# Kernel optimization log

Hardware: AMD Instinct MI355X
Metric: run time of the kernel (lower is better)

## Reference

```python
import jax, jax.numpy as jnp
import numpy as np

HISTORY = 64
WINDOW = 32
DIM = 32
N_PATTERNS = 16
AMP = 2.0


def setup_inputs() -> dict:
    key = jax.random.key(0)
    ks = jax.random.split(key, 7)
    B, L = 128, 131072
    T = L // WINDOW  # 4096 scan steps
    x = jax.random.normal(ks[0], (B, L), jnp.float32)
    avg = jax.random.normal(ks[1], (B, N_PATTERNS), jnp.float32)
    avg_scores = avg - avg.mean(axis=-1, keepdims=True)
    noise = jax.random.normal(ks[2], (B, T, WINDOW), jnp.float32)
    # keys: xavier_uniform on (dim, n_patterns)
    kbound = float(np.sqrt(6.0 / (DIM + N_PATTERNS)))
    keys = jax.random.uniform(ks[3], (DIM, N_PATTERNS), jnp.float32, -kbound, kbound)
    # shapes = rand(n_patterns, 2) * amp * 2
    shapes = jax.random.uniform(ks[4], (N_PATTERNS, 2), jnp.float32) * (AMP * 2.0)
    # conv1d default init: uniform(-1/sqrt(fan_in), 1/sqrt(fan_in)), fan_in = 1*history
    cb = float(1.0 / np.sqrt(HISTORY))
    conv_w = jax.random.uniform(ks[5], (DIM, 1, HISTORY), jnp.float32, -cb, cb)
    conv_b = jax.random.uniform(ks[6], (DIM,), jnp.float32, -cb, cb)
    return {"x": x, "avg_scores": avg_scores, "noise": noise,
            "conv_w": conv_w, "conv_b": conv_b, "keys": keys, "shapes": shapes}


def reference(x, avg_scores, noise, conv_w, conv_b, keys, shapes):
    B, L = x.shape
    inv_p = 1.0 / N_PATTERNS
    # left-pad by history-1, conv1d(1 -> dim, kernel=history, stride=window) + relu
    padded = jnp.pad(x, ((0, 0), (HISTORY - 1, 0)))[:, None, :]  # [B,1,L+H-1]
    out = jax.lax.conv_general_dilated(
        padded, conv_w, window_strides=(WINDOW,), padding='VALID',
        dimension_numbers=('NCH', 'OIH', 'NCH'))  # [B,dim,T]
    out = jax.nn.relu(out + conv_b[None, :, None])
    out = out.transpose(2, 0, 1)  # [T,B,dim]
    # relu6 attention scores against pattern keys
    attn_scores = jnp.clip(jnp.einsum('tbd,dp->tbp', out, keys), 0.0, 6.0)  # [T,B,P]

    def step(avg, score):
        prob = jax.nn.softmax(score - avg, axis=-1)  # [B,P]
        return avg + prob - inv_p, prob

    _, probs = jax.lax.scan(step, avg_scores, attn_scores)  # probs: [T,B,P]
    attn_probs = probs.transpose(1, 0, 2)  # [B,T,P]
    shapeparams = jnp.einsum('btp,pc->btc', attn_probs, shapes)  # [B,T,2]
    offset = shapeparams[:, :, 0:1]  # broadcast over window
    std = shapeparams[:, :, 1:2]
    signal = (offset + noise * std).reshape(B, -1)[:, :L]  # [B,L]
    return jax.nn.relu(signal - x)
```

## Files before the change

### kernel.cpp

```cpp
#include <hip/hip_runtime.h>

static constexpr int BATCH = 128;
static constexpr int LEN   = 131072;
static constexpr int T     = 4096;
static constexpr int DIM   = 32;
static constexpr int NP    = 16;

static constexpr int NCHUNK = 128;
static constexpr int SPC    = T / NCHUNK;
static constexpr int WARM   = 96;

static constexpr int TT = 128;

#define L2E   1.44269504088896340736f
#define L2E16 (1.44269504088896340736f / 16.0f)

typedef __attribute__((ext_vector_type(8))) short  short8;
typedef __attribute__((ext_vector_type(4))) float  f32x4;

__device__ __forceinline__ float fexp2(float x) {
#if __has_builtin(__builtin_amdgcn_exp2f)
  return __builtin_amdgcn_exp2f(x);
#else
  return exp2f(x);
#endif
}

__device__ __forceinline__ float frcp(float x) {
#if __has_builtin(__builtin_amdgcn_rcpf)
  return __builtin_amdgcn_rcpf(x);
#else
  return 1.0f / x;
#endif
}

template <int CTRL>
__device__ __forceinline__ float dppf(float v) {
  return __int_as_float(
      __builtin_amdgcn_update_dpp(0, __float_as_int(v), CTRL, 0xf, 0xf, true));
}

__device__ __forceinline__ float sum16(float v) {
  v += dppf<0xB1>(v);
  v += dppf<0x4E>(v);
  v += dppf<0x141>(v);
  v += dppf<0x140>(v);
  return v;
}

__device__ __forceinline__ short bf16c(float f) {
  unsigned u = __float_as_uint(f);
  unsigned r = u + 0x7fffu + ((u >> 16) & 1u);
  return (short)(r >> 16);
}

__global__ void __launch_bounds__(64) prep_kernel(
    const float* __restrict__ conv_w, const float* __restrict__ conv_b,
    const float* __restrict__ keys, short* __restrict__ frags) {
  int l = threadIdx.x;
  int ln15 = l & 15, kg = l >> 4;
#pragma unroll
  for (int fn = 0; fn < 2; ++fn)
#pragma unroll
    for (int fk = 0; fk < 2; ++fk) {
      const float* wp = conv_w + (fn * 16 + ln15) * 64 + fk * 32 + kg * 8;
      short* dst = frags + ((fn * 2 + fk) * 64 + l) * 8;
#pragma unroll
      for (int j = 0; j < 8; ++j) dst[j] = bf16c(wp[j]);
    }
  short* kd = frags + (256 + l) * 8;
#pragma unroll
  for (int j = 0; j < 8; ++j) kd[j] = bf16c(keys[(kg * 8 + j) * NP + ln15]);
  float* bp = (float*)(frags + 2560);
  bp[2 * l]     = conv_b[ln15];
  bp[2 * l + 1] = conv_b[16 + ln15];
}

__global__ void __launch_bounds__(256) scores_kernel(
    const float* __restrict__ x, const short* __restrict__ frags,
    _Float16* __restrict__ scoresh) {
  __shared__ short lds[4][1728];

  int tid = threadIdx.x;
  int lane = tid & 63;
  int mt   = tid >> 6;
  int blk = blockIdx.x;
  int b  = blk >> 5;
  int bt = blk & 31;
  int t0 = bt * TT;
  int T0w = t0 + mt * 32;
  const float* xb = x + (size_t)b * LEN;
  short* xw = lds[mt];
  short* rl = lds[mt] + 1088;

  int gbase = 32 * T0w - 64 + 16 * lane;
  float f[17];
#pragma unroll
  for (int s = 0; s < 4; ++s) {
    int gi = gbase + 4 * s;
    float4 v = make_float4(0.f, 0.f, 0.f, 0.f);
    if (gi >= 0) v = *(const float4*)(xb + gi);
    f[4 * s]     = v.x; f[4 * s + 1] = v.y;
    f[4 * s + 2] = v.z; f[4 * s + 3] = v.w;
  }
  f[16] = (gbase + 16 >= 0) ? xb[gbase + 16] : 0.f;

  short8 w0, w1;
#pragma unroll
  for (int j = 0; j < 8; ++j) { w0[j] = bf16c(f[j + 1]); w1[j] = bf16c(f[j + 9]); }
  *(short8*)(&xw[16 * lane])     = w0;
  *(short8*)(&xw[16 * lane + 8]) = w1;
  if (lane > 0) xw[16 * lane - 1] = bf16c(f[0]);
  if (lane < 32)
    xw[1024 + lane] = bf16c(xb[32 * T0w + 961 + lane]);

  int ln15 = lane & 15;
  int kg   = lane >> 4;

  const short8* wf = (const short8*)frags;
  short8 bw00 = wf[0 * 64 + lane];
  short8 bw01 = wf[1 * 64 + lane];
  short8 bw10 = wf[2 * 64 + lane];
  short8 bw11 = wf[3 * 64 + lane];
  short8 bk   = wf[4 * 64 + lane];
  const float2* bp = (const float2*)(frags + 2560);
  float2 bias = bp[lane];

  _Float16* dstb = scoresh + (b & 3) * 16 + ln15;

#pragma unroll
  for (int st = 0; st < 2; ++st) {
    int tl = st * 16 + ln15;
    const short* ap = &xw[32 * tl];
    short8 a0 = *(const short8*)(ap + kg * 8);
    short8 a1 = *(const short8*)(ap + 32 + kg * 8);

    f32x4 acc0 = {0.f, 0.f, 0.f, 0.f};
    f32x4 acc1 = {0.f, 0.f, 0.f, 0.f};
    acc0 = __builtin_amdgcn_mfma_f32_16x16x32_bf16(a0, bw00, acc0, 0, 0, 0);
    acc0 = __builtin_amdgcn_mfma_f32_16x16x32_bf16(a1, bw01, acc0, 0, 0, 0);
    acc1 = __builtin_amdgcn_mfma_f32_16x16x32_bf16(a0, bw10, acc1, 0, 0, 0);
    acc1 = __builtin_amdgcn_mfma_f32_16x16x32_bf16(a1, bw11, acc1, 0, 0, 0);

#pragma unroll
    for (int r = 0; r < 4; ++r) {
      int trow = kg * 4 + r;
      rl[trow * 40 + ln15]      = bf16c(fmaxf(acc0[r] + bias.x, 0.f));
      rl[trow * 40 + 16 + ln15] = bf16c(fmaxf(acc1[r] + bias.y, 0.f));
    }
    short8 a2 = *(const short8*)(&rl[ln15 * 40 + kg * 8]);
    f32x4 acc2 = {0.f, 0.f, 0.f, 0.f};
    acc2 = __builtin_amdgcn_mfma_f32_16x16x32_bf16(a2, bk, acc2, 0, 0, 0);

#pragma unroll
    for (int r = 0; r < 4; ++r) {
      float s = fminf(fmaxf(acc2[r], 0.f), 6.f) * L2E;
      int t = T0w + st * 16 + kg * 4 + r;
      dstb[((size_t)(b >> 2) * T + t) * 64] = (_Float16)s;
    }
  }
}

__global__ void __launch_bounds__(256, 8) scanout_kernel(
    const _Float16* __restrict__ scoresh, const float* __restrict__ avg0,
    const float* __restrict__ shapes, const float* __restrict__ x,
    const float* __restrict__ noise, float* __restrict__ out) {
  __shared__ float2 oslds[4][SPC];

  int tid  = threadIdx.x;
  int lane = tid & 63;
  int wid  = tid >> 6;
  int g = blockIdx.x & 31;
  int c = blockIdx.x >> 5;

  size_t base = (size_t)(g * 4) * LEN + (size_t)c * (SPC * 32);
  const float* xp = x     + base + (size_t)wid * LEN + lane * 4;
  const float* np = noise + base + (size_t)wid * LEN + lane * 4;

  f32x4 nv[4];
  if (wid != 0) {
    nv[0] = *(const f32x4*)(np + 0 * 256);
    nv[1] = *(const f32x4*)(np + 1 * 256);
    nv[2] = *(const f32x4*)(np + 2 * 256);
    nv[3] = *(const f32x4*)(np + 3 * 256);
    asm volatile("" :: "v"(nv[0]), "v"(nv[1]), "v"(nv[2]), "v"(nv[3]));
  } else {
    int gid = g * 64 + lane;
    int p = lane & 15;
    int bl = lane >> 4;
    float A = avg0[gid] * L2E;
    float sh0 = shapes[2 * p];
    float sh1 = shapes[2 * p + 1];
    int w = min(WARM, c * SPC);
    int tbeg = c * SPC - w;
    const _Float16* sp = scoresh + ((size_t)g * T + tbeg) * 64 + lane;

    float q0 = (float)sp[0 * 64],  q1 = (float)sp[1 * 64];
    float q2 = (float)sp[2 * 64],  q3 = (float)sp[3 * 64];
    float q4 = (float)sp[4 * 64],  q5 = (float)sp[5 * 64];
    float q6 = (float)sp[6 * 64],  q7 = (float)sp[7 * 64];
    float q8 = (float)sp[8 * 64],  q9 = (float)sp[9 * 64];
    float qa = (float)sp[10 * 64], qb = (float)sp[11 * 64];
    float qc = (float)sp[12 * 64], qd = (float)sp[13 * 64];
    float qe = (float)sp[14 * 64], qf = (float)sp[15 * 64];
    sp += 16 * 64;

#define WSTEP(Q)                                   \
  do {                                             \
    float e = fexp2(Q - A);                        \
    float r = sum16(e);                            \
    A = fmaf(e * L2E, frcp(r), A - L2E16);         \
    Q = (float)sp[0];                              \
    sp += 64;                                      \
  } while (0)

    for (int i = 0; i < w; i += 16) {
      WSTEP(q0); WSTEP(q1); WSTEP(q2); WSTEP(q3);
      WSTEP(q4); WSTEP(q5); WSTEP(q6); WSTEP(q7);
      WSTEP(q8); WSTEP(q9); WSTEP(qa); WSTEP(qb);
      WSTEP(qc); WSTEP(qd); WSTEP(qe); WSTEP(qf);
    }

#define CSTEP(Q, idx)                              \
  do {                                             \
    float e = fexp2(Q - A);                        \
    float r  = sum16(e);                           \
    float u0 = sum16(e * sh0);                     \
    float u1 = sum16(e * sh1);                     \
    float rc = frcp(r);                            \
    A = fmaf(e * L2E, rc, A - L2E16);              \
    if (p == 0) oslds[bl][idx] = make_float2(u0 * rc, u1 * rc); \
    Q = (float)sp[0];                              \
    sp += 64;                                      \
  } while (0)

    for (int i = 0; i < SPC; i += 16) {
      CSTEP(q0, i + 0);  CSTEP(q1, i + 1);  CSTEP(q2, i + 2);  CSTEP(q3, i + 3);
      CSTEP(q4, i + 4);  CSTEP(q5, i + 5);  CSTEP(q6, i + 6);  CSTEP(q7, i + 7);
      CSTEP(q8, i + 8);  CSTEP(q9, i + 9);  CSTEP(qa, i + 10); CSTEP(qb, i + 11);
      CSTEP(qc, i + 12); CSTEP(qd, i + 13); CSTEP(qe, i + 14); CSTEP(qf, i + 15);
    }
#undef WSTEP
#undef CSTEP

    nv[0] = *(const f32x4*)(np + 0 * 256);
    nv[1] = *(const f32x4*)(np + 1 * 256);
    nv[2] = *(const f32x4*)(np + 2 * 256);
    nv[3] = *(const f32x4*)(np + 3 * 256);
  }

  __syncthreads();

  float* op = out + base + (size_t)wid * LEN + lane * 4;
#pragma unroll
  for (int k = 0; k < 4; ++k) {
    f32x4 xv = *(const f32x4*)(xp + k * 256);
    float2 os = oslds[wid][k * 8 + (lane >> 3)];
    f32x4 o;
    o[0] = fmaxf(fmaf(nv[k][0], os.y, os.x) - xv[0], 0.f);
    o[1] = fmaxf(fmaf(nv[k][1], os.y, os.x) - xv[1], 0.f);
    o[2] = fmaxf(fmaf(nv[k][2], os.y, os.x) - xv[2], 0.f);
    o[3] = fmaxf(fmaf(nv[k][3], os.y, os.x) - xv[3], 0.f);
    *(f32x4*)(op + k * 256) = o;
  }
}

extern "C" void kernel_launch(void* const* d_in, const int* in_sizes, int n_in,
                              void* d_out, int out_size, void* d_ws, size_t ws_size,
                              hipStream_t stream) {
  const float* x      = (const float*)d_in[0];
  const float* avg0   = (const float*)d_in[1];
  const float* noise  = (const float*)d_in[2];
  const float* conv_w = (const float*)d_in[3];
  const float* conv_b = (const float*)d_in[4];
  const float* keys   = (const float*)d_in[5];
  const float* shapes = (const float*)d_in[6];
  float* out = (float*)d_out;

  _Float16* scoresh = (_Float16*)d_ws;
  short* frags = (short*)((char*)d_ws + ((size_t)T * BATCH * NP * 2 + 4096));

  prep_kernel<<<1, 64, 0, stream>>>(conv_w, conv_b, keys, frags);
  scores_kernel<<<BATCH * (T / TT), 256, 0, stream>>>(x, frags, scoresh);
  scanout_kernel<<<32 * NCHUNK, 256, 0, stream>>>(scoresh, avg0, shapes, x, noise, out);
}
```

Before: 70.87 us.

## Halve scan chunks and overlap output of first half with second-half scan

Reduces the number of scan chunks from 128 to 64, so each block scans 64 steps and redundant warm-up work per output step is halved. The scan wave splits its steps into two halves. After the first half is in shared memory, the other three waves write their first half of the output while the scan wave computes the second half, then all waves finish after a second barrier. This cuts warm-up overhead and hides part of the serial scan behind memory traffic, at the cost of fewer blocks (less parallelism) and a longer serial chain per block.

```diff
diff --git a/kernel.cpp b/kernel.cpp
--- a/kernel.cpp
+++ b/kernel.cpp
@@ -6,7 +6,7 @@
 static constexpr int DIM   = 32;
 static constexpr int NP    = 16;
 
-static constexpr int NCHUNK = 128;
+static constexpr int NCHUNK = 64;
 static constexpr int SPC    = T / NCHUNK;
 static constexpr int WARM   = 96;
 
@@ -173,37 +173,18 @@
   int g = blockIdx.x & 31;
   int c = blockIdx.x >> 5;
 
-  size_t base = (size_t)(g * 4) * LEN + (size_t)c * (SPC * 32);
+  size_t base = (size_t)(g * 4) * LEN + (size_t)c * 2048;
   const float* xp = x     + base + (size_t)wid * LEN + lane * 4;
   const float* np = noise + base + (size_t)wid * LEN + lane * 4;
+  float*       op = out   + base + (size_t)wid * LEN + lane * 4;
+
+  float A = 0.f, sh0 = 0.f, sh1 = 0.f;
+  float q0, q1, q2, q3, q4, q5, q6, q7, q8, q9, qa, qb, qc, qd, qe, qf;
+  const _Float16* sp = nullptr;
+  int p = lane & 15;
+  int bl = lane >> 4;
 
   f32x4 nv[4];
-  if (wid != 0) {
-    nv[0] = *(const f32x4*)(np + 0 * 256);
-    nv[1] = *(const f32x4*)(np + 1 * 256);
-    nv[2] = *(const f32x4*)(np + 2 * 256);
-    nv[3] = *(const f32x4*)(np + 3 * 256);
-    asm volatile("" :: "v"(nv[0]), "v"(nv[1]), "v"(nv[2]), "v"(nv[3]));
-  } else {
-    int gid = g * 64 + lane;
-    int p = lane & 15;
-    int bl = lane >> 4;
-    float A = avg0[gid] * L2E;
-    float sh0 = shapes[2 * p];
-    float sh1 = shapes[2 * p + 1];
-    int w = min(WARM, c * SPC);
-    int tbeg = c * SPC - w;
-    const _Float16* sp = scoresh + ((size_t)g * T + tbeg) * 64 + lane;
-
-    float q0 = (float)sp[0 * 64],  q1 = (float)sp[1 * 64];
-    float q2 = (float)sp[2 * 64],  q3 = (float)sp[3 * 64];
-    float q4 = (float)sp[4 * 64],  q5 = (float)sp[5 * 64];
-    float q6 = (float)sp[6 * 64],  q7 = (float)sp[7 * 64];
-    float q8 = (float)sp[8 * 64],  q9 = (float)sp[9 * 64];
-    float qa = (float)sp[10 * 64], qb = (float)sp[11 * 64];
-    float qc = (float)sp[12 * 64], qd = (float)sp[13 * 64];
-    float qe = (float)sp[14 * 64], qf = (float)sp[15 * 64];
-    sp += 16 * 64;
 
 #define WSTEP(Q)                                   \
   do {                                             \
@@ -213,13 +194,6 @@
     Q = (float)sp[0];                              \
     sp += 64;                                      \
   } while (0)
-
-    for (int i = 0; i < w; i += 16) {
-      WSTEP(q0); WSTEP(q1); WSTEP(q2); WSTEP(q3);
-      WSTEP(q4); WSTEP(q5); WSTEP(q6); WSTEP(q7);
-      WSTEP(q8); WSTEP(q9); WSTEP(qa); WSTEP(qb);
-      WSTEP(qc); WSTEP(qd); WSTEP(qe); WSTEP(qf);
-    }
 
 #define CSTEP(Q, idx)                              \
   do {                                             \
@@ -234,34 +208,106 @@
     sp += 64;                                      \
   } while (0)
 
-    for (int i = 0; i < SPC; i += 16) {
-      CSTEP(q0, i + 0);  CSTEP(q1, i + 1);  CSTEP(q2, i + 2);  CSTEP(q3, i + 3);
-      CSTEP(q4, i + 4);  CSTEP(q5, i + 5);  CSTEP(q6, i + 6);  CSTEP(q7, i + 7);
-      CSTEP(q8, i + 8);  CSTEP(q9, i + 9);  CSTEP(qa, i + 10); CSTEP(qb, i + 11);
-      CSTEP(qc, i + 12); CSTEP(qd, i + 13); CSTEP(qe, i + 14); CSTEP(qf, i + 15);
-    }
-#undef WSTEP
-#undef CSTEP
-
+  if (wid != 0) {
     nv[0] = *(const f32x4*)(np + 0 * 256);
     nv[1] = *(const f32x4*)(np + 1 * 256);
     nv[2] = *(const f32x4*)(np + 2 * 256);
     nv[3] = *(const f32x4*)(np + 3 * 256);
+    asm volatile("" :: "v"(nv[0]), "v"(nv[1]), "v"(nv[2]), "v"(nv[3]));
+  } else {
+    int gid = g * 64 + lane;
+    A = avg0[gid] * L2E;
+    sh0 = shapes[2 * p];
+    sh1 = shapes[2 * p + 1];
+    int w = min(WARM, c * SPC);
+    int tbeg = c * SPC - w;
+    sp = scoresh + ((size_t)g * T + tbeg) * 64 + lane;
+
+    q0 = (float)sp[0 * 64];  q1 = (float)sp[1 * 64];
+    q2 = (float)sp[2 * 64];  q3 = (float)sp[3 * 64];
+    q4 = (float)sp[4 * 64];  q5 = (float)sp[5 * 64];
+    q6 = (float)sp[6 * 64];  q7 = (float)sp[7 * 64];
+    q8 = (float)sp[8 * 64];  q9 = (float)sp[9 * 64];
+    qa = (float)sp[10 * 64]; qb = (float)sp[11 * 64];
+    qc = (float)sp[12 * 64]; qd = (float)sp[13 * 64];
+    qe = (float)sp[14 * 64]; qf = (float)sp[15 * 64];
+    sp += 16 * 64;
+
+    for (int i = 0; i < w; i += 16) {
+      WSTEP(q0); WSTEP(q1); WSTEP(q2); WSTEP(q3);
+      WSTEP(q4); WSTEP(q5); WSTEP(q6); WSTEP(q7);
+      WSTEP(q8); WSTEP(q9); WSTEP(qa); WSTEP(qb);
+      WSTEP(qc); WSTEP(qd); WSTEP(qe); WSTEP(qf);
+    }
+    CSTEP(q0, 0);  CSTEP(q1, 1);  CSTEP(q2, 2);  CSTEP(q3, 3);
+    CSTEP(q4, 4);  CSTEP(q5, 5);  CSTEP(q6, 6);  CSTEP(q7, 7);
+    CSTEP(q8, 8);  CSTEP(q9, 9);  CSTEP(qa, 10); CSTEP(qb, 11);
+    CSTEP(qc, 12); CSTEP(qd, 13); CSTEP(qe, 14); CSTEP(qf, 15);
+    CSTEP(q0, 16); CSTEP(q1, 17); CSTEP(q2, 18); CSTEP(q3, 19);
+    CSTEP(q4, 20); CSTEP(q5, 21); CSTEP(q6, 22); CSTEP(q7, 23);
+    CSTEP(q8, 24); CSTEP(q9, 25); CSTEP(qa, 26); CSTEP(qb, 27);
+    CSTEP(qc, 28); CSTEP(qd, 29); CSTEP(qe, 30); CSTEP(qf, 31);
   }
 
   __syncthreads();
 
-  float* op = out + base + (size_t)wid * LEN + lane * 4;
-#pragma unroll
-  for (int k = 0; k < 4; ++k) {
-    f32x4 xv = *(const f32x4*)(xp + k * 256);
-    float2 os = oslds[wid][k * 8 + (lane >> 3)];
-    f32x4 o;
-    o[0] = fmaxf(fmaf(nv[k][0], os.y, os.x) - xv[0], 0.f);
-    o[1] = fmaxf(fmaf(nv[k][1], os.y, os.x) - xv[1], 0.f);
-    o[2] = fmaxf(fmaf(nv[k][2], os.y, os.x) - xv[2], 0.f);
-    o[3] = fmaxf(fmaf(nv[k][3], os.y, os.x) - xv[3], 0.f);
-    *(f32x4*)(op + k * 256) = o;
+  if (wid != 0) {
+#pragma unroll
+    for (int k = 0; k < 4; ++k) {
+      f32x4 xv = *(const f32x4*)(xp + k * 256);
+      float2 os = oslds[wid][k * 8 + (lane >> 3)];
+      f32x4 o;
+      o[0] = fmaxf(fmaf(nv[k][0], os.y, os.x) - xv[0], 0.f);
+      o[1] = fmaxf(fmaf(nv[k][1], os.y, os.x) - xv[1], 0.f);
+      o[2] = fmaxf(fmaf(nv[k][2], os.y, os.x) - xv[2], 0.f);
+      o[3] = fmaxf(fmaf(nv[k][3], os.y, os.x) - xv[3], 0.f);
+      *(f32x4*)(op + k * 256) = o;
+    }
+    nv[0] = *(const f32x4*)(np + 4 * 256);
+    nv[1] = *(const f32x4*)(np + 5 * 256);
+    nv[2] = *(const f32x4*)(np + 6 * 256);
+    nv[3] = *(const f32x4*)(np + 7 * 256);
+    asm volatile("" :: "v"(nv[0]), "v"(nv[1]), "v"(nv[2]), "v"(nv[3]));
+  } else {
+    CSTEP(q0, 32); CSTEP(q1, 33); CSTEP(q2, 34); CSTEP(q3, 35);
+    CSTEP(q4, 36); CSTEP(q5, 37); CSTEP(q6, 38); CSTEP(q7, 39);
+    CSTEP(q8, 40); CSTEP(q9, 41); CSTEP(qa, 42); CSTEP(qb, 43);
+    CSTEP(qc, 44); CSTEP(qd, 45); CSTEP(qe, 46); CSTEP(qf, 47);
+    CSTEP(q0, 48); CSTEP(q1, 49); CSTEP(q2, 50); CSTEP(q3, 51);
+    CSTEP(q4, 52); CSTEP(q5, 53); CSTEP(q6, 54); CSTEP(q7, 55);
+    CSTEP(q8, 56); CSTEP(q9, 57); CSTEP(qa, 58); CSTEP(qb, 59);
+    CSTEP(qc, 60); CSTEP(qd, 61); CSTEP(qe, 62); CSTEP(qf, 63);
+  }
+#undef WSTEP
+#undef CSTEP
+
+  __syncthreads();
+
+  if (wid != 0) {
+#pragma unroll
+    for (int k = 4; k < 8; ++k) {
+      f32x4 xv = *(const f32x4*)(xp + k * 256);
+      float2 os = oslds[wid][k * 8 + (lane >> 3)];
+      f32x4 o;
+      o[0] = fmaxf(fmaf(nv[k - 4][0], os.y, os.x) - xv[0], 0.f);
+      o[1] = fmaxf(fmaf(nv[k - 4][1], os.y, os.x) - xv[1], 0.f);
+      o[2] = fmaxf(fmaf(nv[k - 4][2], os.y, os.x) - xv[2], 0.f);
+      o[3] = fmaxf(fmaf(nv[k - 4][3], os.y, os.x) - xv[3], 0.f);
+      *(f32x4*)(op + k * 256) = o;
+    }
+  } else {
+#pragma unroll
+    for (int k = 0; k < 8; ++k) {
+      f32x4 nvv = *(const f32x4*)(np + k * 256);
+      f32x4 xv  = *(const f32x4*)(xp + k * 256);
+      float2 os = oslds[0][k * 8 + (lane >> 3)];
+      f32x4 o;
+      o[0] = fmaxf(fmaf(nvv[0], os.y, os.x) - xv[0], 0.f);
+      o[1] = fmaxf(fmaf(nvv[1], os.y, os.x) - xv[1], 0.f);
+      o[2] = fmaxf(fmaf(nvv[2], os.y, os.x) - xv[2], 0.f);
+      o[3] = fmaxf(fmaf(nvv[3], os.y, os.x) - xv[3], 0.f);
+      *(f32x4*)(op + k * 256) = o;
+    }
   }
 }
 
```

After: 68.54 us. 1.03x faster.
